# Optimization experiments

Measured on AMD Instinct MI355X. Metric: run time of the kernel, lower is better.

## Reference

```python
import jax, jax.numpy as jnp
import numpy as np

Z_SIZE, X_SIZE = 7, 14
B, H, C = 64, 12, 768
N = Z_SIZE * Z_SIZE + X_SIZE * X_SIZE  # 245
HEAD_DIM = C // H
SCALE = HEAD_DIM ** -0.5


def _build_rel_idx():
    # 2D concatenated (template+search) relative position index
    zh, zw = np.meshgrid(np.arange(Z_SIZE), np.arange(Z_SIZE), indexing='ij')
    xh, xw = np.meshgrid(np.arange(X_SIZE), np.arange(X_SIZE), indexing='ij')
    hh = np.concatenate([zh.ravel(), xh.ravel()])
    ww = np.concatenate([zw.ravel(), xw.ravel()])
    flag = np.concatenate([np.zeros(Z_SIZE * Z_SIZE), np.ones(X_SIZE * X_SIZE)])
    dh = hh[:, None] - hh[None, :]
    dw = ww[:, None] - ww[None, :]
    fa = np.broadcast_to(flag[:, None], dh.shape)
    fb = np.broadcast_to(flag[None, :], dh.shape)
    key = np.stack([dh, dw, fa, fb], axis=-1).reshape(-1, 4)
    uniq, inv = np.unique(key, axis=0, return_inverse=True)
    return inv.reshape(N, N).astype(np.int32), uniq.shape[0]


def setup_inputs() -> dict:
    key = jax.random.key(0)
    ks = jax.random.split(key, 9)
    rel_idx_np, n_buckets = _build_rel_idx()  # n_buckets == 1698
    std = 0.02
    return {
        'x': jax.random.normal(ks[0], (B, N, C), jnp.float32),
        'w_qkv': jax.random.normal(ks[1], (3 * C, C), jnp.float32) * std,
        'w_proj': jax.random.normal(ks[2], (C, C), jnp.float32) * std,
        'b_proj': jnp.zeros((C,), jnp.float32),
        'w_l': jax.random.normal(ks[3], (H, H), jnp.float32) * std + jnp.eye(H),
        'b_l': jnp.zeros((H,), jnp.float32),
        'w_w': jax.random.normal(ks[4], (H, H), jnp.float32) * std + jnp.eye(H),
        'b_w': jnp.zeros((H,), jnp.float32),
        'rpe_table': jax.random.normal(ks[5], (H, n_buckets), jnp.float32) * std,
        'rel_idx': jnp.asarray(rel_idx_np),
    }


def reference(x, w_qkv, w_proj, b_proj, w_l, b_l, w_w, b_w, rpe_table, rel_idx):
    b, n, c = x.shape
    h, d = H, c // H
    qkv = jnp.einsum('bnc,ec->bne', x, w_qkv).reshape(b, n, 3, h, d)
    qkv = jnp.transpose(qkv, (2, 0, 3, 1, 4))  # (3, B, H, N, D)
    q, k, v = qkv[0] * SCALE, qkv[1], qkv[2]
    attn = jnp.einsum('bhnd,bhmd->bhnm', q, k)  # (B,H,N,N)
    # RPE bias: table[:, rel_idx] -> (H, N, N)
    attn = attn + rpe_table[:, rel_idx][None]
    # talking heads pre-softmax: Linear over head dim (out = attn_h @ W^T + b)
    attn = jnp.einsum('bhnm,gh->bgnm', attn, w_l) + b_l[None, :, None, None]
    attn = jax.nn.softmax(attn, axis=-1)
    # talking heads post-softmax
    attn = jnp.einsum('bhnm,gh->bgnm', attn, w_w) + b_w[None, :, None, None]
    out = jnp.einsum('bhnm,bhmd->bnhd', attn, v).reshape(b, n, c)
    out = jnp.einsum('bnc,oc->bno', out, w_proj) + b_proj
    return out
```

## Files before the change

### kernel.cpp

```cpp
#include <hip/hip_runtime.h>
#include <hip/hip_bf16.h>

#define NN 245
#define NP 256
#define HH 12
#define DD 64
#define CC 768
#define NBUCKET 1698
#define MROWS (64 * NN)

typedef __bf16 bf16x8 __attribute__((ext_vector_type(8)));
typedef float f32x4 __attribute__((ext_vector_type(4)));

#define MFMA(a, b, c) __builtin_amdgcn_mfma_f32_16x16x32_bf16(a, b, c, 0, 0, 0)

static __device__ __forceinline__ f32x4 fzero() {
    f32x4 z = {0.f, 0.f, 0.f, 0.f};
    return z;
}

static __device__ __forceinline__ bf16x8 cvt8(f32x4 lo, f32x4 hi) {
    bf16x8 r;
    #pragma unroll
    for (int i = 0; i < 4; ++i) { r[i] = (__bf16)lo[i]; r[i + 4] = (__bf16)hi[i]; }
    return r;
}

static __device__ __forceinline__ void gl_lds16(const __bf16* g, __bf16* l) {
    __builtin_amdgcn_global_load_lds(
        (const __attribute__((address_space(1))) void*)g,
        (__attribute__((address_space(3))) void*)l, 16, 0, 0);
}

__global__ __launch_bounds__(256) void prep(
    const float* __restrict__ x,     __bf16* __restrict__ xb,
    const float* __restrict__ wqkv,  __bf16* __restrict__ wb,
    const float* __restrict__ wproj, __bf16* __restrict__ wpb,
    const float* __restrict__ rpe, const int* __restrict__ relidx,
    const float* __restrict__ wl_, const float* __restrict__ bl_,
    __bf16* __restrict__ biasb, __bf16* __restrict__ VT)
{
    __shared__ float wl[144];
    __shared__ float bl[12];
    int bid = blockIdx.x, t = threadIdx.x;

    if (bid < 2048) {
        const int n8 = MROWS * CC / 8;
        int i = bid * 256 + t;
        int stride = 2048 * 256;
        for (; i < n8; i += stride) {
            f32x4 a = *(const f32x4*)(x + (size_t)i * 8);
            f32x4 b = *(const f32x4*)(x + (size_t)i * 8 + 4);
            *(bf16x8*)(xb + (size_t)i * 8) = cvt8(a, b);
        }
    } else if (bid < 2912) {
        int i = (bid - 2048) * 256 + t;
        f32x4 a = *(const f32x4*)(wqkv + (size_t)i * 8);
        f32x4 b = *(const f32x4*)(wqkv + (size_t)i * 8 + 4);
        *(bf16x8*)(wb + (size_t)i * 8) = cvt8(a, b);
    } else if (bid < 3200) {
        int i = (bid - 2912) * 256 + t;
        f32x4 a = *(const f32x4*)(wproj + (size_t)i * 8);
        f32x4 b = *(const f32x4*)(wproj + (size_t)i * 8 + 4);
        *(bf16x8*)(wpb + (size_t)i * 8) = cvt8(a, b);
    } else if (bid < 3456) {
        if (t < 144) wl[t] = wl_[t];
        if (t < 12)  bl[t] = bl_[t];
        __syncthreads();
        int n = bid - 3200;
        int m = t;
        float r[12];
        bool valid = (n < NN) && (m < NN);
        if (valid) {
            int idx = relidx[n * NN + m];
            #pragma unroll
            for (int h = 0; h < 12; ++h) r[h] = rpe[h * NBUCKET + idx];
        }
        #pragma unroll
        for (int g = 0; g < 12; ++g) {
            float o = -30000.f;
            if (valid) {
                o = bl[g];
                #pragma unroll
                for (int h = 0; h < 12; ++h) o += wl[g * 12 + h] * r[h];
            }
            biasb[(size_t)(g * 256 + n) * 256 + m] = (__bf16)o;
        }
    } else {
        int row = (bid - 3456) * 256 + t;
        __bf16* p = VT + (size_t)row * NP + NN;
        __bf16 z = (__bf16)0.f;
        #pragma unroll
        for (int j = 0; j < 11; ++j) p[j] = z;
    }
}

template<int EPI>
__global__ __launch_bounds__(256) void gemm128(
    const __bf16* __restrict__ A, const __bf16* __restrict__ Bw,
    __bf16* __restrict__ Q, __bf16* __restrict__ Kb, __bf16* __restrict__ VT,
    const float* __restrict__ bproj, float* __restrict__ outp)
{
    __shared__ __attribute__((aligned(16))) __bf16 sA[128 * 32];
    __shared__ __attribute__((aligned(16))) __bf16 sB[128 * 32];
    int tid = threadIdx.x, lane = tid & 63, wave = tid >> 6;

    int gx = gridDim.x;
    int nwg = gx * gridDim.y;
    int wg = blockIdx.y * gx + blockIdx.x;
    int q8 = nwg >> 3, r8 = nwg & 7;
    int xcd = wg & 7, idx = wg >> 3;
    int swz = (xcd < r8 ? xcd * (q8 + 1) : r8 * (q8 + 1) + (xcd - r8) * q8) + idx;
    int et = swz % gx, mt = swz / gx;
    int m0 = mt * 128, e0 = et * 128;

    int r1 = tid >> 2, chunk = tid & 3;
    int gar1 = m0 + r1;        if (gar1 >= MROWS) gar1 = MROWS - 1;
    int gar2 = m0 + 64 + r1;   if (gar2 >= MROWS) gar2 = MROWS - 1;
    const __bf16* aA1 = A  + (size_t)gar1 * CC + chunk * 8;
    const __bf16* aA2 = A  + (size_t)gar2 * CC + chunk * 8;
    const __bf16* aB1 = Bw + (size_t)(e0 + r1) * CC + chunk * 8;
    const __bf16* aB2 = Bw + (size_t)(e0 + 64 + r1) * CC + chunk * 8;
    __bf16* lA1 = sA + tid * 8;
    __bf16* lA2 = sA + tid * 8 + 2048;
    __bf16* lB1 = sB + tid * 8;
    __bf16* lB2 = sB + tid * 8 + 2048;

    int wr = wave >> 1, wc = wave & 1;
    int lrow = lane & 15, lk = (lane >> 4) * 8;
    const __bf16* ra = sA + (wr * 64 + lrow) * 32 + lk;
    const __bf16* rb = sB + (wc * 64 + lrow) * 32 + lk;

    f32x4 acc[4][4];
    #pragma unroll
    for (int q = 0; q < 4; ++q)
        #pragma unroll
        for (int n = 0; n < 4; ++n) acc[q][n] = fzero();

    for (int it = 0; it < 24; ++it) {
        __syncthreads();
        gl_lds16(aA1 + it * 32, lA1);
        gl_lds16(aA2 + it * 32, lA2);
        gl_lds16(aB1 + it * 32, lB1);
        gl_lds16(aB2 + it * 32, lB2);
        __syncthreads();
        bf16x8 af[4], bfr[4];
        #pragma unroll
        for (int q = 0; q < 4; ++q) af[q]  = *(const bf16x8*)(ra + q * 512);
        #pragma unroll
        for (int n = 0; n < 4; ++n) bfr[n] = *(const bf16x8*)(rb + n * 512);
        #pragma unroll
        for (int q = 0; q < 4; ++q)
            #pragma unroll
            for (int n = 0; n < 4; ++n)
                acc[q][n] = MFMA(af[q], bfr[n], acc[q][n]);
    }

    int col = lane & 15, rbs = (lane >> 4) * 4;
    #pragma unroll
    for (int q = 0; q < 4; ++q) {
        int gmb = m0 + wr * 64 + q * 16 + rbs;
        #pragma unroll
        for (int n = 0; n < 4; ++n) {
            int e = e0 + wc * 64 + n * 16 + col;
            if (EPI == 0) {
                int which = e / CC;
                int h = (e % CC) >> 6;
                int d = e & 63;
                #pragma unroll
                for (int r = 0; r < 4; ++r) {
                    int gm = gmb + r;
                    if (gm < MROWS) {
                        int bidx = gm / NN, nn = gm - bidx * NN;
                        float v = acc[q][n][r];
                        if (which == 0)
                            Q[((size_t)(bidx * 12 + h) * NP + nn) * 64 + d] = (__bf16)(v * 0.125f);
                        else if (which == 1)
                            Kb[((size_t)(bidx * 12 + h) * NP + nn) * 64 + d] = (__bf16)v;
                        else
                            VT[((size_t)(bidx * 12 + h) * 64 + d) * NP + nn] = (__bf16)v;
                    }
                }
            } else {
                float bv = bproj[e];
                #pragma unroll
                for (int r = 0; r < 4; ++r) {
                    int gm = gmb + r;
                    if (gm < MROWS)
                        outp[(size_t)gm * CC + e] = acc[q][n][r] + bv;
                }
            }
        }
    }
}

__global__ __launch_bounds__(512, 4) void k2c_qk(
    const __bf16* __restrict__ Q, const __bf16* __restrict__ Kb,
    const __bf16* __restrict__ biasb, const float* __restrict__ wl_,
    __bf16* __restrict__ S)
{
    __shared__ float wl[144];
    int tid = threadIdx.x, wave = tid >> 6, lane = tid & 63;
    if (tid < 144) wl[tid] = wl_[tid];
    __syncthreads();

    int wg = blockIdx.x;
    int L = (wg & 7) * 256 + (wg >> 3);
    int b = L >> 5, rem = L & 31;
    int mq = rem & 3, nt = rem >> 2;
    int wn = wave >> 2, wm = wave & 3;
    int n0 = nt * 32 + wn * 16;
    int m0 = mq * 64 + wm * 16;

    int lrow = lane & 15, lk = (lane >> 4) * 8;
    f32x4 acc[12];
    #pragma unroll
    for (int h = 0; h < 12; ++h) acc[h] = fzero();
    #pragma unroll
    for (int h = 0; h < 12; ++h) {
        const __bf16* qb = Q  + ((size_t)(b * 12 + h) * NP + n0 + lrow) * 64 + lk;
        const __bf16* kb = Kb + ((size_t)(b * 12 + h) * NP + m0 + lrow) * 64 + lk;
        bf16x8 a0 = *(const bf16x8*)qb;
        bf16x8 b0 = *(const bf16x8*)kb;
        bf16x8 a1 = *(const bf16x8*)(qb + 32);
        bf16x8 b1 = *(const bf16x8*)(kb + 32);
        acc[h] = MFMA(a0, b0, acc[h]);
        acc[h] = MFMA(a1, b1, acc[h]);
    }
    int col = lane & 15, rb = (lane >> 4) * 4;
    #pragma unroll
    for (int g = 0; g < 12; ++g) {
        f32x4 s = fzero();
        #pragma unroll
        for (int h = 0; h < 12; ++h) {
            float w = wl[g * 12 + h];
            s += acc[h] * w;
        }
        #pragma unroll
        for (int r = 0; r < 4; ++r) {
            int n = n0 + rb + r;
            int m = m0 + col;
            float v = s[r] + (float)biasb[(size_t)(g * 256 + n) * 256 + m];
            S[((size_t)(b * 12 + g) * NP + n) * NP + m] = (__bf16)v;
        }
    }
}

__global__ __launch_bounds__(512, 3) void k34_smx_pv(
    const __bf16* __restrict__ S, const __bf16* __restrict__ VT,
    const float* __restrict__ ww_, const float* __restrict__ bw_,
    __bf16* __restrict__ aout)
{
    __shared__ __attribute__((aligned(16))) __bf16 Pp[2][16][264];
    __shared__ float ww[144];
    __shared__ float bw[12];
    int tid = threadIdx.x;
    if (tid < 144) ww[tid] = ww_[tid];
    if (tid >= 256 && tid < 268) bw[tid - 256] = bw_[tid - 256];

    int W = blockIdx.x;
    int g8 = W & 7, kk = W >> 3;
    int L = (kk >> 4) * 128 + g8 * 16 + (kk & 15);
    int b = L >> 4, nt = L & 15;
    int n0 = nt * 16;

    int n = tid >> 5, ms = tid & 31;
    int lane = tid & 63, wave = tid >> 6;

    float P[12][8];
    #pragma unroll
    for (int g = 0; g < 12; ++g) {
        const __bf16* rowp = S + ((size_t)(b * 12 + g) * NP + n0 + n) * NP + ms * 8;
        bf16x8 sv = *(const bf16x8*)rowp;
        float v[8];
        float mx = -1e30f;
        #pragma unroll
        for (int j = 0; j < 8; ++j) {
            v[j] = (ms * 8 + j < NN) ? (float)sv[j] : -1e30f;
            mx = fmaxf(mx, v[j]);
        }
        #pragma unroll
        for (int o = 16; o > 0; o >>= 1) mx = fmaxf(mx, __shfl_xor(mx, o));
        float sum = 0.f;
        #pragma unroll
        for (int j = 0; j < 8; ++j) {
            float e = (ms * 8 + j < NN) ? __expf(v[j] - mx) : 0.f;
            P[g][j] = e;
            sum += e;
        }
        #pragma unroll
        for (int o = 16; o > 0; o >>= 1) sum += __shfl_xor(sum, o);
        float inv = 1.f / sum;
        #pragma unroll
        for (int j = 0; j < 8; ++j) P[g][j] *= inv;
    }
    __syncthreads();

    int dt = wave >> 1, wgp = wave & 1;
    int lrow = lane & 15, lk = (lane >> 4) * 8;
    int col = lane & 15, rb = (lane >> 4) * 4;
    #pragma unroll
    for (int c = 0; c < 6; ++c) {
        #pragma unroll
        for (int gi = 0; gi < 2; ++gi) {
            int gp = c * 2 + gi;
            bf16x8 o;
            #pragma unroll
            for (int j = 0; j < 8; ++j) {
                float a = bw[gp];
                #pragma unroll
                for (int g = 0; g < 12; ++g) a += ww[gp * 12 + g] * P[g][j];
                o[j] = (__bf16)((ms * 8 + j < NN) ? a : 0.f);
            }
            *(bf16x8*)&Pp[gi][n][ms * 8] = o;
        }
        __syncthreads();
        int gp = c * 2 + wgp;
        f32x4 acc = fzero();
        const __bf16* vb = VT + ((size_t)(b * 12 + gp) * 64 + dt * 16 + lrow) * NP + lk;
        #pragma unroll
        for (int kt = 0; kt < 8; ++kt) {
            bf16x8 av = *(const bf16x8*)&Pp[wgp][lrow][kt * 32 + lk];
            bf16x8 bv = *(const bf16x8*)(vb + kt * 32);
            acc = MFMA(av, bv, acc);
        }
        #pragma unroll
        for (int r = 0; r < 4; ++r) {
            int gn = n0 + rb + r;
            if (gn < NN)
                aout[((size_t)b * NN + gn) * CC + gp * 64 + dt * 16 + col] = (__bf16)acc[r];
        }
        __syncthreads();
    }
}

extern "C" void kernel_launch(void* const* d_in, const int* in_sizes, int n_in,
                              void* d_out, int out_size, void* d_ws, size_t ws_size,
                              hipStream_t stream)
{
    (void)in_sizes; (void)n_in; (void)out_size; (void)ws_size;
    const float* x     = (const float*)d_in[0];
    const float* wqkv  = (const float*)d_in[1];
    const float* wproj = (const float*)d_in[2];
    const float* bproj = (const float*)d_in[3];
    const float* wl    = (const float*)d_in[4];
    const float* bl    = (const float*)d_in[5];
    const float* ww    = (const float*)d_in[6];
    const float* bw    = (const float*)d_in[7];
    const float* rpe   = (const float*)d_in[8];
    const int*   rel   = (const int*)d_in[9];

    char* ws = (char*)d_ws;
    const size_t SZ_QKV = (size_t)64 * 12 * 256 * 64 * 2;
    const size_t SZ_S   = (size_t)64 * 12 * 256 * 256 * 2;
    __bf16* Q     = (__bf16*)(ws);
    __bf16* Kb    = (__bf16*)(ws + SZ_QKV);
    __bf16* VT    = (__bf16*)(ws + 2 * SZ_QKV);
    __bf16* biasb = (__bf16*)(ws + 3 * SZ_QKV);
    char*   sreg  = ws + 3 * SZ_QKV + (size_t)12 * 256 * 256 * 4;
    __bf16* S     = (__bf16*)sreg;
    __bf16* xb    = (__bf16*)sreg;
    __bf16* wb    = (__bf16*)(sreg + (size_t)MROWS * CC * 2);
    __bf16* wpb   = (__bf16*)(ws + 3 * SZ_QKV + (size_t)12 * 256 * 256 * 4 + SZ_S);
    __bf16* aout  = Q;

    prep<<<dim3(3648), 256, 0, stream>>>(x, xb, wqkv, wb, wproj, wpb,
                                         rpe, rel, wl, bl, biasb, VT);
    gemm128<0><<<dim3(18, 123), 256, 0, stream>>>(xb, wb, Q, Kb, VT, nullptr, nullptr);
    k2c_qk<<<dim3(2048), 512, 0, stream>>>(Q, Kb, biasb, wl, S);
    k34_smx_pv<<<dim3(1024), 512, 0, stream>>>(S, VT, ww, bw, aout);
    gemm128<1><<<dim3(6, 123), 256, 0, stream>>>(aout, wpb, nullptr, nullptr, nullptr,
                                                 bproj, (float*)d_out);
}
```

Measured before the change: 361.2 us.

## Double-buffer LDS tiles in gemm128 to overlap global loads with MFMA

Converts the single-buffered K-loop of the bf16 GEMM into a two-stage pipeline: two LDS buffers per operand, prefetching tile it+2 while computing tile it, with explicit vmcnt waits, raw s_barrier and sched_barrier fences. This targets the exposed global-to-LDS load latency that the previous sync-load-sync-compute loop serialized. It doubles LDS use per block (32KB), which may reduce occupancy, and relies on hand-placed waitcnt counts that must match the number of outstanding loads.

```diff
diff --git a/kernel.cpp b/kernel.cpp
--- a/kernel.cpp
+++ b/kernel.cpp
@@ -101,8 +101,8 @@
     __bf16* __restrict__ Q, __bf16* __restrict__ Kb, __bf16* __restrict__ VT,
     const float* __restrict__ bproj, float* __restrict__ outp)
 {
-    __shared__ __attribute__((aligned(16))) __bf16 sA[128 * 32];
-    __shared__ __attribute__((aligned(16))) __bf16 sB[128 * 32];
+    __shared__ __attribute__((aligned(16))) __bf16 sA[2][128 * 32];
+    __shared__ __attribute__((aligned(16))) __bf16 sB[2][128 * 32];
     int tid = threadIdx.x, lane = tid & 63, wave = tid >> 6;
 
     int gx = gridDim.x;
@@ -121,15 +121,12 @@
     const __bf16* aA2 = A  + (size_t)gar2 * CC + chunk * 8;
     const __bf16* aB1 = Bw + (size_t)(e0 + r1) * CC + chunk * 8;
     const __bf16* aB2 = Bw + (size_t)(e0 + 64 + r1) * CC + chunk * 8;
-    __bf16* lA1 = sA + tid * 8;
-    __bf16* lA2 = sA + tid * 8 + 2048;
-    __bf16* lB1 = sB + tid * 8;
-    __bf16* lB2 = sB + tid * 8 + 2048;
+    int off = tid * 8;
 
     int wr = wave >> 1, wc = wave & 1;
     int lrow = lane & 15, lk = (lane >> 4) * 8;
-    const __bf16* ra = sA + (wr * 64 + lrow) * 32 + lk;
-    const __bf16* rb = sB + (wc * 64 + lrow) * 32 + lk;
+    int roff = (wr * 64 + lrow) * 32 + lk;
+    int boff = (wc * 64 + lrow) * 32 + lk;
 
     f32x4 acc[4][4];
     #pragma unroll
@@ -137,24 +134,62 @@
         #pragma unroll
         for (int n = 0; n < 4; ++n) acc[q][n] = fzero();
 
-    for (int it = 0; it < 24; ++it) {
-        __syncthreads();
-        gl_lds16(aA1 + it * 32, lA1);
-        gl_lds16(aA2 + it * 32, lA2);
-        gl_lds16(aB1 + it * 32, lB1);
-        gl_lds16(aB2 + it * 32, lB2);
-        __syncthreads();
-        bf16x8 af[4], bfr[4];
-        #pragma unroll
-        for (int q = 0; q < 4; ++q) af[q]  = *(const bf16x8*)(ra + q * 512);
-        #pragma unroll
-        for (int n = 0; n < 4; ++n) bfr[n] = *(const bf16x8*)(rb + n * 512);
-        #pragma unroll
-        for (int q = 0; q < 4; ++q)
-            #pragma unroll
-            for (int n = 0; n < 4; ++n)
-                acc[q][n] = MFMA(af[q], bfr[n], acc[q][n]);
-    }
+    #define STAGE(s, t) do {                                   \
+        gl_lds16(aA1 + (t) * 32, &sA[s][off]);                 \
+        gl_lds16(aA2 + (t) * 32, &sA[s][off + 2048]);          \
+        gl_lds16(aB1 + (t) * 32, &sB[s][off]);                 \
+        gl_lds16(aB2 + (t) * 32, &sB[s][off + 2048]);          \
+    } while (0)
+
+    #define COMPUTE(s) do {                                    \
+        bf16x8 af[4], bfr[4];                                  \
+        _Pragma("unroll")                                      \
+        for (int q = 0; q < 4; ++q)                            \
+            af[q]  = *(const bf16x8*)(&sA[s][roff + q * 512]); \
+        _Pragma("unroll")                                      \
+        for (int n = 0; n < 4; ++n)                            \
+            bfr[n] = *(const bf16x8*)(&sB[s][boff + n * 512]); \
+        _Pragma("unroll")                                      \
+        for (int q = 0; q < 4; ++q)                            \
+            _Pragma("unroll")                                  \
+            for (int n = 0; n < 4; ++n)                        \
+                acc[q][n] = MFMA(af[q], bfr[n], acc[q][n]);    \
+    } while (0)
+
+    #define SBAR()   asm volatile("s_barrier" ::: "memory")
+    #define VMCNT(n) asm volatile("s_waitcnt vmcnt(" #n ")" ::: "memory")
+    #define LGKM0()  asm volatile("s_waitcnt lgkmcnt(0)" ::: "memory")
+    #define SCHED0() __builtin_amdgcn_sched_barrier(0)
+
+    STAGE(0, 0);
+    STAGE(1, 1);
+    VMCNT(4);
+    SBAR();
+    SCHED0();
+
+    for (int it = 0; it < 23; ++it) {
+        int s = it & 1;
+        COMPUTE(s);
+        LGKM0();
+        SCHED0();
+        SBAR();
+        if (it + 2 < 24) {
+            STAGE(s, it + 2);
+            VMCNT(4);
+        } else {
+            VMCNT(0);
+        }
+        SBAR();
+        SCHED0();
+    }
+    COMPUTE(1);
+
+    #undef STAGE
+    #undef COMPUTE
+    #undef SBAR
+    #undef VMCNT
+    #undef LGKM0
+    #undef SCHED0
 
     int col = lane & 15, rbs = (lane >> 4) * 4;
     #pragma unroll
```

Result: no change. 362.8 us (+0.4%).

## Stage Q/K tiles through double-buffered LDS in QK kernel

Applied to the files above, without the earlier changes.

The QK-logits kernel now loads each head's 32x64 Q tile and 64x64 K tile cooperatively into a double-buffered shared-memory tile, using padded rows. Each wave then reads its MFMA fragments from LDS instead of every wave issuing its own redundant global loads. The next head's global loads are prefetched into registers while the current head computes. This cuts duplicated global/L2 traffic across the 8 waves, at the cost of a block-wide barrier per head and extra LDS use, which may reduce occupancy.

```diff
diff --git a/kernel.cpp b/kernel.cpp
--- a/kernel.cpp
+++ b/kernel.cpp
@@ -199,34 +199,63 @@
     const __bf16* __restrict__ biasb, const float* __restrict__ wl_,
     __bf16* __restrict__ S)
 {
+    __shared__ __attribute__((aligned(16))) __bf16 sT[2][96 * 72];
     __shared__ float wl[144];
     int tid = threadIdx.x, wave = tid >> 6, lane = tid & 63;
     if (tid < 144) wl[tid] = wl_[tid];
-    __syncthreads();
 
     int wg = blockIdx.x;
     int L = (wg & 7) * 256 + (wg >> 3);
     int b = L >> 5, rem = L & 31;
     int mq = rem & 3, nt = rem >> 2;
     int wn = wave >> 2, wm = wave & 3;
-    int n0 = nt * 32 + wn * 16;
-    int m0 = mq * 64 + wm * 16;
+    int n0b = nt * 32, m0b = mq * 64;
+    int n0 = n0b + wn * 16;
+    int m0 = m0b + wm * 16;
+
+    bool hasQ = (tid < 256);
+    int kc = hasQ ? (tid + 256) : (tid - 256);
+    int qsrc = (n0b + (tid >> 3)) * 64 + (tid & 7) * 8;
+    int qdst = (tid >> 3) * 72 + (tid & 7) * 8;
+    int ksrc = (m0b + (kc >> 3)) * 64 + (kc & 7) * 8;
+    int kdst = (32 + (kc >> 3)) * 72 + (kc & 7) * 8;
 
     int lrow = lane & 15, lk = (lane >> 4) * 8;
+    int aR = (wn * 16 + lrow) * 72 + lk;
+    int bR = (32 + wm * 16 + lrow) * 72 + lk;
+
     f32x4 acc[12];
     #pragma unroll
     for (int h = 0; h < 12; ++h) acc[h] = fzero();
+
+    size_t hb = (size_t)(b * 12) << 14;
+    bf16x8 rk = *(const bf16x8*)(Kb + hb + ksrc);
+    bf16x8 rq;
+    if (hasQ) rq = *(const bf16x8*)(Q + hb + qsrc);
+    *(bf16x8*)&sT[0][kdst] = rk;
+    if (hasQ) *(bf16x8*)&sT[0][qdst] = rq;
+
     #pragma unroll
     for (int h = 0; h < 12; ++h) {
-        const __bf16* qb = Q  + ((size_t)(b * 12 + h) * NP + n0 + lrow) * 64 + lk;
-        const __bf16* kb = Kb + ((size_t)(b * 12 + h) * NP + m0 + lrow) * 64 + lk;
-        bf16x8 a0 = *(const bf16x8*)qb;
-        bf16x8 b0 = *(const bf16x8*)kb;
-        bf16x8 a1 = *(const bf16x8*)(qb + 32);
-        bf16x8 b1 = *(const bf16x8*)(kb + 32);
+        int s = h & 1;
+        if (h < 11) {
+            size_t hb2 = (size_t)(b * 12 + h + 1) << 14;
+            rk = *(const bf16x8*)(Kb + hb2 + ksrc);
+            if (hasQ) rq = *(const bf16x8*)(Q + hb2 + qsrc);
+        }
+        __syncthreads();
+        bf16x8 a0 = *(const bf16x8*)&sT[s][aR];
+        bf16x8 a1 = *(const bf16x8*)&sT[s][aR + 32];
+        bf16x8 b0 = *(const bf16x8*)&sT[s][bR];
+        bf16x8 b1 = *(const bf16x8*)&sT[s][bR + 32];
         acc[h] = MFMA(a0, b0, acc[h]);
         acc[h] = MFMA(a1, b1, acc[h]);
-    }
+        if (h < 11) {
+            *(bf16x8*)&sT[s ^ 1][kdst] = rk;
+            if (hasQ) *(bf16x8*)&sT[s ^ 1][qdst] = rq;
+        }
+    }
+
     int col = lane & 15, rb = (lane >> 4) * 4;
     #pragma unroll
     for (int g = 0; g < 12; ++g) {
```

Measured after the change: 313.4 us. -13.2%, faster.
